# Optimization experiments

Hardware: AMD Instinct MI355X
Metric: run time of the kernel (lower is better)

## Reference

```python
import jax, jax.numpy as jnp
import numpy as np

NEG = -9.0e15
D = 768


def _init_params(key, d):
    ks = jax.random.split(key, 12)
    s = 0.02
    p = {}
    p['Wa'] = jax.random.normal(ks[0], (d, 1), jnp.float32) * s
    p['ba'] = jnp.zeros((1,), jnp.float32)
    for i, name in enumerate(['qs', 'ks', 'qc', 'kc', 'qr', 'kr']):
        p['W' + name] = jax.random.normal(ks[1 + i], (d, d), jnp.float32) * s
        p['b' + name] = jnp.zeros((d,), jnp.float32)
    p['Wf1'] = jax.random.normal(ks[8], (3 * d, d), jnp.float32) * s
    p['bf1'] = jnp.zeros((d,), jnp.float32)
    p['Wf2'] = jax.random.normal(ks[9], (d, d), jnp.float32) * s
    p['bf2'] = jnp.zeros((d,), jnp.float32)
    p['gamma'] = jnp.ones((d,), jnp.float32)
    p['beta'] = jnp.zeros((d,), jnp.float32)
    return p


def setup_inputs() -> dict:
    key = jax.random.key(0)
    k1, k2, k3 = jax.random.split(key, 3)
    B, L = 8, 1024
    inp = {
        'x': jax.random.normal(k1, (B, L, D), jnp.float32),
        'x_ids': jax.random.randint(k2, (B, L), 0, 1000, jnp.int64 if jax.config.read('jax_enable_x64') else jnp.int32).astype(jnp.int32),
        'pad_idx': 0,
    }
    inp.update(_init_params(k3, D))
    return inp


def _forward(x, x_ids, pad_idx, Wa, ba, Wqs, bqs, Wks, bks, Wqc, bqc, Wkc, bkc,
             Wqr, bqr, Wkr, bkr, Wf1, bf1, Wf2, bf2, gamma, beta):
    B, L, d = x.shape
    valid = x_ids != pad_idx                             # [B,L]
    valid_len = valid.sum(axis=1)
    sep_pos = jnp.clip(valid_len // 2, 1, max(1, L - 2))  # [B]
    pos = jnp.arange(L)[None, :]                          # [1,L]
    false_mask = (pos < sep_pos[:, None]) & valid         # [B,L]
    option_mask = (pos > sep_pos[:, None]) & valid        # [B,L]

    # anomaly gate over false segment
    a_logits = (x @ Wa + ba)[..., 0]                      # [B,L]
    a_logits = jnp.where(false_mask, a_logits, NEG)
    gate = jax.nn.softmax(a_logits, axis=1) * false_mask.astype(x.dtype)
    gate = gate / jnp.clip(gate.sum(axis=1, keepdims=True), 1e-8)

    scale = 1.0 / jnp.sqrt(jnp.asarray(d, x.dtype))
    q_sup, k_sup = x @ Wqs + bqs, x @ Wks + bks
    q_con, k_con = x @ Wqc + bqc, x @ Wkc + bkc
    q_rep, k_rep = x @ Wqr + bqr, x @ Wkr + bkr

    sup_s = jnp.einsum('bld,bmd->blm', q_sup, k_sup) * scale
    con_s = jnp.einsum('bld,bmd->blm', q_con, k_con) * scale
    rep_s = jnp.einsum('bld,bmd->blm', q_rep, k_rep) * scale

    pair_mask = false_mask[:, :, None] & option_mask[:, None, :]  # [B,L,L]
    sup_attn = jax.nn.softmax(jnp.where(pair_mask, sup_s, NEG), axis=-1)
    rep_attn = jax.nn.softmax(jnp.where(pair_mask, rep_s + jnp.tanh(con_s), NEG), axis=-1)

    rep_vec = jnp.einsum('blm,bmd->bld', rep_attn, x)
    sup_vec = jnp.einsum('blm,bmd->bld', sup_attn, x)

    anomaly_false = jnp.einsum('bl,bld->bd', gate, x)
    w_rep = jnp.einsum('bl,bld->bd', gate, rep_vec)
    w_sup = jnp.einsum('bl,bld->bd', gate, sup_vec)

    fused = jnp.concatenate([anomaly_false, w_rep, w_sup], axis=-1)
    fused = jnp.maximum(fused @ Wf1 + bf1, 0.0) @ Wf2 + bf2  # dropout = eval identity

    mu = fused.mean(axis=-1, keepdims=True)
    var = ((fused - mu) ** 2).mean(axis=-1, keepdims=True)
    fused = (fused - mu) / jnp.sqrt(var + 1e-5) * gamma + beta
    return fused


def reference(x, x_ids, pad_idx, Wa, ba, Wqs, bqs, Wks, bks, Wqc, bqc, Wkc, bkc,
              Wqr, bqr, Wkr, bkr, Wf1, bf1, Wf2, bf2, gamma, beta):
    return _forward(x, x_ids, pad_idx, Wa, ba, Wqs, bqs, Wks, bks, Wqc, bqc,
                    Wkc, bkc, Wqr, bqr, Wkr, bkr, Wf1, bf1, Wf2, bf2, gamma, beta)
```

## Files before the change

### kernel.cpp

```cpp
#include <hip/hip_runtime.h>
#include <math.h>

#define L 1024
#define NB 8
#define D 768
#define NEGV (-9.0e15f)
#define SCALE 0.036084391824351615f

typedef unsigned short u16;
typedef __attribute__((ext_vector_type(8))) short short8;
typedef __attribute__((ext_vector_type(4))) float float4v;
#define MFMA_BF16 __builtin_amdgcn_mfma_f32_16x16x32_bf16

__device__ __forceinline__ float b2f(u16 u) {
    union { unsigned int i; float f; } v; v.i = ((unsigned int)u) << 16; return v.f;
}
__device__ __forceinline__ u16 f2b(float f) {
    union { float fv; unsigned int i; } v; v.fv = f;
    unsigned int x = v.i;
    x += 0x7fffu + ((x >> 16) & 1u);
    return (u16)(x >> 16);
}
__device__ __forceinline__ float unpk(unsigned int w, int h) {
    return b2f((u16)(h ? (w >> 16) : (w & 0xffffu)));
}

template<int F32>
__device__ __forceinline__ float4 ld4(const void* p, size_t idx) {
    if (F32) return *(const float4*)((const float*)p + idx);
    ushort4 v = *(const ushort4*)((const u16*)p + idx);
    return make_float4(b2f(v.x), b2f(v.y), b2f(v.z), b2f(v.w));
}
template<int F32>
__device__ __forceinline__ float ld1(const void* p, size_t idx) {
    if (F32) return ((const float*)p)[idx];
    return b2f(((const u16*)p)[idx]);
}
__device__ __forceinline__ int ldid(const int* p, size_t idx, int is64) {
    return is64 ? p[idx * 2] : p[idx];
}

__device__ __forceinline__ void detect2(const void* x, const void* ids, int* sh) {
    int tid = threadIdx.x;
    if (tid < 64) {
        u16 u = ((const u16*)x)[tid * 2];
        int e = (u >> 7) & 0xFF;
        unsigned long long balf = __ballot(e >= 100 && e <= 140);
        int v = ((const int*)ids)[tid * 2 + 1];
        unsigned long long bali = __ballot(v != 0);
        if (tid == 0) {
            sh[0] = (__popcll(balf) < 32) ? 1 : 0;
            sh[1] = (bali == 0ULL) ? 1 : 0;
        }
    }
    __syncthreads();
}

#define WS_FLAG  ((size_t)0)
#define WS_SEP   ((size_t)64)
#define WS_C0    ((size_t)128)
#define WS_Z0    ((size_t)192)
#define WS_W1    ((size_t)9472)
#define WS_GATE  ((size_t)18752)
#define WS_CSUP  ((size_t)51520)
#define WS_CREP  ((size_t)84288)
#define WS_AF    ((size_t)117056)
#define WS_WREP  ((size_t)141632)
#define WS_WSUP  ((size_t)166208)
#define WS_HACC  ((size_t)190784)
#define WS_ALOG  ((size_t)215360)
#define WS_T     ((size_t)248128)
#define WS_OACC  ((size_t)303104)
#define WS_XB    ((size_t)524288)
#define WS_Z     ((size_t)13107200)
#define WS_WB    ((size_t)31981568)
#define WS_M     ((size_t)40370176)

struct PP { const void* W[6]; const void* b[6]; };

template<int F32> __device__ void kbias_body(const void* W, const void* vec,
        float* out, float* vs, int xi) {
    int tid = threadIdx.x;
    for (int i = tid; i < D; i += 256) vs[i] = ld1<F32>(vec, i);
    __syncthreads();
    int row = xi * 64 + (tid >> 2);
    int sub = tid & 3;
    float acc = 0.f;
    for (int i = 0; i < 48; ++i) {
        int k = i * 16 + sub * 4;
        float4 wv = ld4<F32>(W, (size_t)row * D + k);
        acc += wv.x * vs[k] + wv.y * vs[k + 1] + wv.z * vs[k + 2] + wv.w * vs[k + 3];
    }
    acc += __shfl_xor(acc, 1);
    acc += __shfl_xor(acc, 2);
    if (sub == 0) out[row] = acc;
}
template<int F32> __device__ void kc0_body(const void* bq, const void* bk,
        float* c0, float* red) {
    int tid = threadIdx.x;
    float s = 0.f;
    for (int i = tid; i < D; i += 256) s += ld1<F32>(bq, i) * ld1<F32>(bk, i);
    red[tid] = s; __syncthreads();
    for (int st = 128; st > 0; st >>= 1) { if (tid < st) red[tid] += red[tid + st]; __syncthreads(); }
    if (tid == 0) c0[0] = red[0];
}

template<int F32> __device__ void kx_body(const void* x, const void* Wa,
        const void* ba, u16* xb, float* alog, float* ws2) {
    int tid = threadIdx.x;
    for (int i = tid; i < D; i += 256) ws2[i] = ld1<F32>(Wa, i);
    __syncthreads();
    int row = blockIdx.x * 32 + (tid >> 3);
    int sub = tid & 7;
    float a0 = 0.f;
    for (int i = 0; i < 24; ++i) {
        int k = i * 32 + sub * 4;
        float4 xv = ld4<F32>(x, (size_t)row * D + k);
        ushort4 o;
        o.x = f2b(xv.x); o.y = f2b(xv.y); o.z = f2b(xv.z); o.w = f2b(xv.w);
        *(ushort4*)(xb + (size_t)row * D + k) = o;
        a0 += xv.x * ws2[k] + xv.y * ws2[k + 1] + xv.z * ws2[k + 2] + xv.w * ws2[k + 3];
    }
    #pragma unroll
    for (int d = 1; d < 8; d <<= 1) a0 += __shfl_xor(a0, d);
    if (sub == 0) alog[row] = a0 + ld1<F32>(ba, 0);
}
__global__ __launch_bounds__(256) void kx(const void* x, const int* ids, PP pp,
        const void* Wa, const void* ba, u16* xb, u16* Wb, float* alog,
        float* z0, float* w1, float* c0f) {
    __shared__ float sf[2 * D];
    __shared__ int fsh[2];
    detect2(x, ids, fsh);
    int F32 = fsh[0];
    int bid = blockIdx.x;
    if (bid < 256) {
        if (F32) kx_body<1>(x, Wa, ba, xb, alog, sf);
        else     kx_body<0>(x, Wa, ba, xb, alog, sf);
        return;
    }
    if (bid < 1984) {
        int t = (bid - 256) / 288, inner = (bid - 256) % 288;
        const void* src = pp.W[t];
        u16* dst = Wb + (size_t)t * D * D;
        size_t base = ((size_t)inner * 256 + threadIdx.x) * 8;
        if (F32) {
            float4 a = *(const float4*)((const float*)src + base);
            float4 b = *(const float4*)((const float*)src + base + 4);
            uint4 o; u16* po = (u16*)&o;
            po[0] = f2b(a.x); po[1] = f2b(a.y); po[2] = f2b(a.z); po[3] = f2b(a.w);
            po[4] = f2b(b.x); po[5] = f2b(b.y); po[6] = f2b(b.z); po[7] = f2b(b.w);
            *(uint4*)(dst + base) = o;
        } else {
            *(uint4*)(dst + base) = *(const uint4*)((const u16*)src + base);
        }
        return;
    }
    int i = bid - 1984;
    int y = i / 12, xi = i % 12;
    float* vs = sf;
    float* red = sf + D;
    if (y == 4) {
        if (xi != 0) return;
        if (F32) kc0_body<1>(pp.b[2], pp.b[3], c0f, red);
        else     kc0_body<0>(pp.b[2], pp.b[3], c0f, red);
        return;
    }
    const void* W; const void* vec; float* out;
    if (y < 3) { W = pp.W[2 * y + 1]; vec = pp.b[2 * y]; out = z0 + y * D; }
    else       { W = pp.W[2];         vec = pp.b[3];     out = w1; }
    if (F32) kbias_body<1>(W, vec, out, vs, xi);
    else     kbias_body<0>(W, vec, out, vs, xi);
}

__device__ __forceinline__ void stage128_async(const u16* __restrict__ G, size_t ld,
        int r0, int k0, u16* S, int tid) {
    int rowa = tid >> 2;
    int koa = ((tid & 3) ^ (rowa & 3)) << 3;
    int wave = tid >> 6;
    const u16* g1 = &G[(size_t)(r0 + rowa) * ld + k0 + koa];
    const u16* g2 = &G[(size_t)(r0 + rowa + 64) * ld + k0 + koa];
    __builtin_amdgcn_global_load_lds((__attribute__((address_space(1))) void*)(u16*)g1,
        (__attribute__((address_space(3))) void*)(S + wave * 512), 16, 0, 0);
    __builtin_amdgcn_global_load_lds((__attribute__((address_space(1))) void*)(u16*)g2,
        (__attribute__((address_space(3))) void*)(S + 2048 + wave * 512), 16, 0, 0);
}
__device__ __forceinline__ void stage64_async(const u16* __restrict__ G, size_t ld,
        int r0, int k0, u16* S, int tid) {
    int rowa = tid >> 2;
    int koa = ((tid & 3) ^ (rowa & 3)) << 3;
    int wave = tid >> 6;
    const u16* g = &G[(size_t)(r0 + rowa) * ld + k0 + koa];
    __builtin_amdgcn_global_load_lds((__attribute__((address_space(1))) void*)(u16*)g,
        (__attribute__((address_space(3))) void*)(S + wave * 512), 16, 0, 0);
}

__device__ __forceinline__ void gemm64_cnt(const u16* __restrict__ A, size_t lda, int r0,
        const u16* __restrict__ B, size_t ldb, int c0,
        u16* As, u16* Bs, float4v acc[2][4]) {
    int tid = threadIdx.x;
    int lane = tid & 63, wave = tid >> 6;
    int wm = (wave >> 1) << 5, wn = (wave & 1) << 6;
    int quad = lane >> 4, lrow = lane & 15;
    int sq = ((quad ^ (lrow & 3)) << 3);
    #pragma unroll
    for (int i = 0; i < 2; ++i)
        #pragma unroll
        for (int j = 0; j < 4; ++j) acc[i][j] = (float4v){0.f, 0.f, 0.f, 0.f};
    stage64_async(A, lda, r0, 0, As, tid);
    stage64_async(A, lda, r0, 32, As + 2048, tid);
    stage128_async(B, ldb, c0, 0, Bs, tid);
    stage128_async(B, ldb, c0, 32, Bs + 4096, tid);
    stage64_async(A, lda, r0, 64, As + 4096, tid);
    stage64_async(A, lda, r0, 96, As + 6144, tid);
    stage128_async(B, ldb, c0, 64, Bs + 8192, tid);
    stage128_async(B, ldb, c0, 96, Bs + 12288, tid);
    #pragma unroll 1
    for (int t = 0; t < 12; ++t) {
        int cur = t & 1;
        if (t != 11) asm volatile("s_waitcnt vmcnt(6)" ::: "memory");
        else         asm volatile("s_waitcnt vmcnt(0)" ::: "memory");
        __builtin_amdgcn_s_barrier();
        const u16* Ab = As + cur * 4096;
        const u16* Bb = Bs + cur * 8192;
        short8 fa[2][2], fb[2][4];
        #pragma unroll
        for (int p = 0; p < 2; ++p) {
            #pragma unroll
            for (int i = 0; i < 2; ++i)
                fa[p][i] = *(const short8*)&Ab[p * 2048 + (wm + i * 16 + lrow) * 32 + sq];
            #pragma unroll
            for (int j = 0; j < 4; ++j)
                fb[p][j] = *(const short8*)&Bb[p * 4096 + (wn + j * 16 + lrow) * 32 + sq];
        }
        asm volatile("s_waitcnt lgkmcnt(0)" ::: "memory");
        __builtin_amdgcn_sched_barrier(0);
        __builtin_amdgcn_s_barrier();
        if (t < 10) {
            int k0 = (t + 2) << 6;
            u16* Ad = As + cur * 4096;
            u16* Bd = Bs + cur * 8192;
            stage64_async(A, lda, r0, k0, Ad, tid);
            stage64_async(A, lda, r0, k0 + 32, Ad + 2048, tid);
            stage128_async(B, ldb, c0, k0, Bd, tid);
            stage128_async(B, ldb, c0, k0 + 32, Bd + 4096, tid);
        }
        #pragma unroll
        for (int p = 0; p < 2; ++p)
            #pragma unroll
            for (int i = 0; i < 2; ++i)
                #pragma unroll
                for (int j = 0; j < 4; ++j)
                    acc[i][j] = MFMA_BF16(fa[p][i], fb[p][j], acc[i][j], 0, 0, 0);
    }
}

__device__ __forceinline__ void gemm128_cnt(const u16* __restrict__ A, size_t lda, int r0,
        const u16* __restrict__ B, size_t ldb, int c0,
        u16* As, u16* Bs, float4v acc[4][4]) {
    int tid = threadIdx.x;
    int lane = tid & 63, wave = tid >> 6;
    int wm = (wave >> 1) << 6, wn = (wave & 1) << 6;
    int quad = lane >> 4, lrow = lane & 15;
    int sq = ((quad ^ (lrow & 3)) << 3);
    #pragma unroll
    for (int i = 0; i < 4; ++i)
        #pragma unroll
        for (int j = 0; j < 4; ++j) acc[i][j] = (float4v){0.f, 0.f, 0.f, 0.f};
    stage128_async(A, lda, r0, 0, As, tid);
    stage128_async(A, lda, r0, 32, As + 4096, tid);
    stage128_async(B, ldb, c0, 0, Bs, tid);
    stage128_async(B, ldb, c0, 32, Bs + 4096, tid);
    stage128_async(A, lda, r0, 64, As + 8192, tid);
    stage128_async(A, lda, r0, 96, As + 12288, tid);
    stage128_async(B, ldb, c0, 64, Bs + 8192, tid);
    stage128_async(B, ldb, c0, 96, Bs + 12288, tid);
    #pragma unroll 1
    for (int t = 0; t < 12; ++t) {
        int cur = t & 1;
        if (t != 11) asm volatile("s_waitcnt vmcnt(8)" ::: "memory");
        else         asm volatile("s_waitcnt vmcnt(0)" ::: "memory");
        __builtin_amdgcn_s_barrier();
        const u16* Ab = As + cur * 8192;
        const u16* Bb = Bs + cur * 8192;
        short8 fa[2][4], fb[2][4];
        #pragma unroll
        for (int p = 0; p < 2; ++p) {
            #pragma unroll
            for (int i = 0; i < 4; ++i)
                fa[p][i] = *(const short8*)&Ab[p * 4096 + (wm + i * 16 + lrow) * 32 + sq];
            #pragma unroll
            for (int j = 0; j < 4; ++j)
                fb[p][j] = *(const short8*)&Bb[p * 4096 + (wn + j * 16 + lrow) * 32 + sq];
        }
        asm volatile("s_waitcnt lgkmcnt(0)" ::: "memory");
        __builtin_amdgcn_sched_barrier(0);
        __builtin_amdgcn_s_barrier();
        if (t < 10) {
            int k0 = (t + 2) << 6;
            u16* Ad = As + cur * 8192;
            u16* Bd = Bs + cur * 8192;
            stage128_async(A, lda, r0, k0, Ad, tid);
            stage128_async(A, lda, r0, k0 + 32, Ad + 4096, tid);
            stage128_async(B, ldb, c0, k0, Bd, tid);
            stage128_async(B, ldb, c0, k0 + 32, Bd + 4096, tid);
        }
        #pragma unroll
        for (int p = 0; p < 2; ++p)
            #pragma unroll
            for (int i = 0; i < 4; ++i)
                #pragma unroll
                for (int j = 0; j < 4; ++j)
                    acc[i][j] = MFMA_BF16(fa[p][i], fb[p][j], acc[i][j], 0, 0, 0);
    }
}

__global__ __launch_bounds__(256) void kB(const void* x, const int* __restrict__ ids,
        const int* __restrict__ padp, const float* __restrict__ alog,
        float* __restrict__ gate, int* __restrict__ sepArr,
        float* __restrict__ af, float* __restrict__ wrep, float* __restrict__ wsup,
        float* __restrict__ hacc, float* __restrict__ oacc,
        float* __restrict__ csup, float* __restrict__ crep,
        const u16* __restrict__ xb, const float* __restrict__ w1,
        const float* __restrict__ c0f, float* __restrict__ tbuf,
        const u16* __restrict__ Wb, u16* __restrict__ Mt) {
    __shared__ __align__(16) u16 SMEM[24576];
    int bid = blockIdx.x;
    int tid = threadIdx.x;
    if (bid >= 8 && bid < 224) {
        int i = bid - 8;
        int p = i / 72, j = i % 72;
        int r0 = (j / 6) * 64, c0m = (j % 6) * 128;
        u16* As = SMEM;
        u16* Bs = SMEM + 8192;
        float4v acc[2][4];
        gemm64_cnt(Wb + (size_t)(2 * p + 1) * D * D, D, r0,
                   Wb + (size_t)(2 * p) * D * D, D, c0m, As, Bs, acc);
        int lane = tid & 63, wave = tid >> 6;
        int wm = (wave >> 1) << 5, wn = (wave & 1) << 6;
        int quad = lane >> 4, lrow = lane & 15;
        u16* out = Mt + (size_t)p * D * D;
        #pragma unroll
        for (int ii = 0; ii < 2; ++ii)
            #pragma unroll
            for (int jj = 0; jj < 4; ++jj) {
                int brow = r0 + wm + ii * 16 + quad * 4;
                int col = c0m + wn + jj * 16 + lrow;
                #pragma unroll
                for (int r = 0; r < 4; ++r)
                    out[(size_t)(brow + r) * D + col] = f2b(acc[ii][jj][r]);
            }
        return;
    }
    if (bid >= 224) {
        int i = bid - 224;
        int b = i >> 2, q = i & 3;
        float* w1s = (float*)SMEM;
        for (int j = tid; j < D; j += 256) w1s[j] = w1[j];
        __syncthreads();
        float c0v = c0f[0];
        int sub = tid & 15;
        int rowi = tid >> 4;
        for (int pass = 0; pass < 8; ++pass) {
            int l = q * 128 + pass * 16 + rowi;
            const u16* xr = xb + ((size_t)b * L + l) * D;
            float a = 0.f;
            #pragma unroll
            for (int i2 = 0; i2 < 6; ++i2) {
                int k = i2 * 128 + sub * 8;
                short8 v = *(const short8*)&xr[k];
                #pragma unroll
                for (int e = 0; e < 8; ++e) a += b2f((u16)v[e]) * w1s[k + e];
            }
            #pragma unroll
            for (int d2 = 1; d2 < 16; d2 <<= 1) a += __shfl_xor(a, d2);
            if (sub == 0) tbuf[b * 512 + l] = a + c0v;
        }
        return;
    }
    float* red = (float*)SMEM;
    int*   ish = (int*)(red + 256);
    detect2(x, ids, ish);
    int is64 = ish[1];
    int b = bid;
    int pad = padp[0];
    int cnt = 0;
    for (int l = tid; l < L; l += 256) cnt += (ldid(ids, (size_t)b * L + l, is64) != pad) ? 1 : 0;
    red[tid] = (float)cnt; __syncthreads();
    for (int s = 128; s > 0; s >>= 1) { if (tid < s) red[tid] += red[tid + s]; __syncthreads(); }
    if (tid == 0) {
        int vl = (int)red[0];
        int sep = vl / 2; if (sep < 1) sep = 1; if (sep > L - 2) sep = L - 2;
        ish[2] = sep; sepArr[b] = sep;
    }
    __syncthreads();
    int sep = ish[2];
    float lv[4]; int lidx[4];
    float mx = -3.4e38f;
    for (int u = 0; u < 4; ++u) {
        int l = tid + u * 256; lidx[u] = l;
        bool fm = (l < sep) && (ldid(ids, (size_t)b * L + l, is64) != pad);
        float v = fm ? alog[b * L + l] : NEGV;
        lv[u] = v; mx = fmaxf(mx, v);
    }
    red[tid] = mx; __syncthreads();
    for (int s = 128; s > 0; s >>= 1) { if (tid < s) red[tid] = fmaxf(red[tid], red[tid + s]); __syncthreads(); }
    mx = red[0]; __syncthreads();
    float se = 0.f;
    for (int u = 0; u < 4; ++u) { lv[u] = expf(lv[u] - mx); se += lv[u]; }
    red[tid] = se; __syncthreads();
    for (int s = 128; s > 0; s >>= 1) { if (tid < s) red[tid] += red[tid + s]; __syncthreads(); }
    float den = fmaxf(red[0], 1e-30f); __syncthreads();
    float gs = 0.f; float gv[4];
    for (int u = 0; u < 4; ++u) {
        int l = lidx[u];
        bool fm = (l < sep) && (ldid(ids, (size_t)b * L + l, is64) != pad);
        float p = lv[u] / den;
        gv[u] = fm ? p : 0.f;
        gs += gv[u];
    }
    red[tid] = gs; __syncthreads();
    for (int s = 128; s > 0; s >>= 1) { if (tid < s) red[tid] += red[tid + s]; __syncthreads(); }
    gs = red[0];
    float inv = 1.f / fmaxf(gs, 1e-8f);
    for (int u = 0; u < 4; ++u) gate[b * L + lidx[u]] = gv[u] * inv;
    for (int l = tid; l < L; l += 256) { csup[b * L + l] = 0.f; crep[b * L + l] = 0.f; }
    for (int i = tid; i < D; i += 256) {
        af[b * D + i] = 0.f; wrep[b * D + i] = 0.f; wsup[b * D + i] = 0.f;
        hacc[b * D + i] = 0.f; oacc[b * D + i] = 0.f;
    }
}

__global__ __launch_bounds__(256) void kZ_mfma(const u16* __restrict__ xb,
        const u16* __restrict__ Mt, const float* __restrict__ z0,
        u16* __restrict__ Zbuf, const int* __restrict__ sepArr) {
    __shared__ __align__(16) u16 As[16384];
    __shared__ __align__(16) u16 Bs[16384];
    int z = blockIdx.z;
    int p = z >> 3, b = z & 7;
    int sep = sepArr[b];
    int r0 = blockIdx.y * 128;
    if (r0 >= sep) return;
    int c0 = blockIdx.x * 128;
    float4v acc[4][4];
    gemm128_cnt(xb + (size_t)b * L * D, D, r0,
                Mt + (size_t)p * D * D, D, c0, As, Bs, acc);
    int lane = threadIdx.x & 63, wave = threadIdx.x >> 6;
    int wm = (wave >> 1) << 6, wn = (wave & 1) << 6;
    int quad = lane >> 4, lrow = lane & 15;
    const float* z0p = z0 + p * D;
    u16* out = Zbuf + ((size_t)p * NB + b) * 512 * D;
    #pragma unroll
    for (int i = 0; i < 4; ++i)
        #pragma unroll
        for (int j = 0; j < 4; ++j) {
            int brow = r0 + wm + i * 16 + quad * 4;
            int col = c0 + wn + j * 16 + lrow;
            float zb = z0p[col];
            #pragma unroll
            for (int r = 0; r < 4; ++r)
                out[(size_t)(brow + r) * D + col] = f2b(acc[i][j][r] + zb);
        }
}

__global__ __launch_bounds__(512) void kS2(const u16* __restrict__ Zbuf,
        const u16* __restrict__ xb, const float* __restrict__ tcbuf,
        const int* __restrict__ sepArr, const int* __restrict__ ids,
        const int* __restrict__ padp, const float* __restrict__ gate,
        float* __restrict__ csup, float* __restrict__ crep) {
    __shared__ __align__(16) u16 Alds[24576];
    __shared__ float redmx[2][8][16];
    __shared__ float redsm[2][8][16];
    __shared__ int ish[1];
    int bid = blockIdx.x;
    int b = bid & 7;
    int l0 = (bid >> 3) * 16;
    int sep = sepArr[b];
    int tid = threadIdx.x, lane = tid & 63, wave = tid >> 6;
    int lrow = lane & 15, quad = lane >> 4;
    if (tid < 64) {
        int v = ((const int*)ids)[tid * 2 + 1];
        unsigned long long bali = __ballot(v != 0);
        if (tid == 0) ish[0] = (bali == 0ULL) ? 1 : 0;
    }
    __syncthreads();
    if (l0 >= sep) return;
    int is64 = ish[0];
    int pad = padp[0];
    int msta = ((sep + 1) >> 7) << 7;
    int nchunk = (L - msta) >> 7;
    const u16* A0 = Zbuf + (size_t)b * 512 * D;
    const u16* A1 = Zbuf + ((size_t)NB + b) * 512 * D;
    const u16* A2 = Zbuf + ((size_t)2 * NB + b) * 512 * D;
    const u16* X  = xb + (size_t)b * L * D;
    #pragma unroll
    for (int i = 0; i < 6; ++i) {
        int s = tid + i * 512;
        int m = s / 1536, rem = s - m * 1536;
        int r = rem / 96, c = rem - r * 96;
        const u16* src = (m == 0 ? A1 : A2) + (size_t)(l0 + r) * D + c * 8;
        *(short8*)&Alds[(((m * 16 + r) * 96) + (c ^ (r & 7))) * 8] = *(const short8*)src;
    }
    __syncthreads();
    float tcv[4], gr[4];
    #pragma unroll
    for (int r = 0; r < 4; ++r) {
        tcv[r] = tcbuf[b * 512 + l0 + quad * 4 + r];
        gr[r]  = gate[b * L + l0 + quad * 4 + r];
    }
    int xr = lrow & 7;
    int arow0 = lrow * 768;
    const u16* pA0_ = A0 + (size_t)(l0 + lrow) * D + quad * 8;
    unsigned int pS[8][2], pC[8][2];
    #pragma unroll
    for (int g = 0; g < 2; ++g) {
      if (g * 4 < nchunk) {
        const u16 *pB0_, *pB1_, *pB2_, *pB3_;
        {
            int m00 = msta + (g * 4 + 0) * 128; if (m00 > L - 128) m00 = L - 128;
            int m01 = msta + (g * 4 + 1) * 128; if (m01 > L - 128) m01 = L - 128;
            int m02 = msta + (g * 4 + 2) * 128; if (m02 > L - 128) m02 = L - 128;
            int m03 = msta + (g * 4 + 3) * 128; if (m03 > L - 128) m03 = L - 128;
            pB0_ = X + (size_t)(m00 + wave * 16 + lrow) * D + quad * 8;
            pB1_ = X + (size_t)(m01 + wave * 16 + lrow) * D + quad * 8;
            pB2_ = X + (size_t)(m02 + wave * 16 + lrow) * D + quad * 8;
            pB3_ = X + (size_t)(m03 + wave * 16 + lrow) * D + quad * 8;
        }
        float4v acc[3][4];
        #pragma unroll
        for (int m = 0; m < 3; ++m)
            #pragma unroll
            for (int cc = 0; cc < 4; ++cc) acc[m][cc] = (float4v){0.f, 0.f, 0.f, 0.f};
        short8 fA1, fA2;
        short8 A0a, B0a, B1a, B2a, B3a;
        short8 A0b, B0b, B1b, B2b, B3b;
        short8 A0c, B0c, B1c, B2c, B3c;
#define GL_(dst, base, imm) asm volatile("global_load_dwordx4 %0, %1, off offset:" #imm : "=v"(dst) : "v"(base))
#define GL(dst, base, imm) GL_(dst, base, imm)
#define LDG5(SUF, IMM) do { \
        GL(A0##SUF, pA0_, IMM); \
        GL(B0##SUF, pB0_, IMM); GL(B1##SUF, pB1_, IMM); \
        GL(B2##SUF, pB2_, IMM); GL(B3##SUF, pB3_, IMM); } while (0)
#define LDA(S) do { int sw = (((4 * (S) + quad) ^ xr) << 3); \
        fA1 = *(const short8*)&Alds[arow0 + sw]; \
        fA2 = *(const short8*)&Alds[12288 + arow0 + sw]; } while (0)
#define WAITN_(N) do { asm volatile("s_waitcnt vmcnt(" #N ")"); \
        __builtin_amdgcn_sched_barrier(0); } while (0)
#define WAITN(N) WAITN_(N)
#define CPSTEP(SUF) do { \
        acc[0][0] = MFMA_BF16(A0##SUF, B0##SUF, acc[0][0], 0, 0, 0); \
        acc[1][0] = MFMA_BF16(fA1, B0##SUF, acc[1][0], 0, 0, 0); \
        acc[2][0] = MFMA_BF16(fA2, B0##SUF, acc[2][0], 0, 0, 0); \
        acc[0][1] = MFMA_BF16(A0##SUF, B1##SUF, acc[0][1], 0, 0, 0); \
        acc[1][1] = MFMA_BF16(fA1, B1##SUF, acc[1][1], 0, 0, 0); \
        acc[2][1] = MFMA_BF16(fA2, B1##SUF, acc[2][1], 0, 0, 0); \
        acc[0][2] = MFMA_BF16(A0##SUF, B2##SUF, acc[0][2], 0, 0, 0); \
        acc[1][2] = MFMA_BF16(fA1, B2##SUF, acc[1][2], 0, 0, 0); \
        acc[2][2] = MFMA_BF16(fA2, B2##SUF, acc[2][2], 0, 0, 0); \
        acc[0][3] = MFMA_BF16(A0##SUF, B3##SUF, acc[0][3], 0, 0, 0); \
        acc[1][3] = MFMA_BF16(fA1, B3##SUF, acc[1][3], 0, 0, 0); \
        acc[2][3] = MFMA_BF16(fA2, B3##SUF, acc[2][3], 0, 0, 0); } while (0)
        WAITN(0);
        LDG5(a, 0); LDG5(b, 64); LDG5(c, 128);
        LDA(0);  WAITN(10); CPSTEP(a); LDG5(a, 192);
        LDA(1);  WAITN(10); CPSTEP(b); LDG5(b, 256);
        LDA(2);  WAITN(10); CPSTEP(c); LDG5(c, 320);
        LDA(3);  WAITN(10); CPSTEP(a); LDG5(a, 384);
        LDA(4);  WAITN(10); CPSTEP(b); LDG5(b, 448);
        LDA(5);  WAITN(10); CPSTEP(c); LDG5(c, 512);
        LDA(6);  WAITN(10); CPSTEP(a); LDG5(a, 576);
        LDA(7);  WAITN(10); CPSTEP(b); LDG5(b, 640);
        LDA(8);  WAITN(10); CPSTEP(c); LDG5(c, 704);
        LDA(9);  WAITN(10); CPSTEP(a); LDG5(a, 768);
        LDA(10); WAITN(10); CPSTEP(b); LDG5(b, 832);
        LDA(11); WAITN(10); CPSTEP(c); LDG5(c, 896);
        LDA(12); WAITN(10); CPSTEP(a); LDG5(a, 960);
        LDA(13); WAITN(10); CPSTEP(b); LDG5(b, 1024);
        LDA(14); WAITN(10); CPSTEP(c); LDG5(c, 1088);
        LDA(15); WAITN(10); CPSTEP(a); LDG5(a, 1152);
        LDA(16); WAITN(10); CPSTEP(b); LDG5(b, 1216);
        LDA(17); WAITN(10); CPSTEP(c); LDG5(c, 1280);
        LDA(18); WAITN(10); CPSTEP(a); LDG5(a, 1344);
        LDA(19); WAITN(10); CPSTEP(b); LDG5(b, 1408);
        LDA(20); WAITN(10); CPSTEP(c); LDG5(c, 1472);
        LDA(21); WAITN(10); CPSTEP(a);
        LDA(22); WAITN(5);  CPSTEP(b);
        LDA(23); WAITN(0);  CPSTEP(c);
#undef GL_
#undef GL
#undef LDG5
#undef LDA
#undef WAITN_
#undef WAITN
#undef CPSTEP
        #pragma unroll
        for (int cc = 0; cc < 4; ++cc) {
            int c = g * 4 + cc;
            if (c < nchunk) {
                int m = msta + c * 128 + wave * 16 + lrow;
                bool ok = (m > sep) && (ldid(ids, (size_t)b * L + m, is64) != pad);
                float vs[4], vc[4];
                #pragma unroll
                for (int r = 0; r < 4; ++r) {
                    vs[r] = ok ? acc[0][cc][r] * SCALE : NEGV;
                    vc[r] = ok ? (acc[2][cc][r] * SCALE
                                  + tanhf((acc[1][cc][r] + tcv[r]) * SCALE)) : NEGV;
                }
                pS[c][0] = (unsigned)f2b(vs[0]) | ((unsigned)f2b(vs[1]) << 16);
                pS[c][1] = (unsigned)f2b(vs[2]) | ((unsigned)f2b(vs[3]) << 16);
                pC[c][0] = (unsigned)f2b(vc[0]) | ((unsigned)f2b(vc[1]) << 16);
                pC[c][1] = (unsigned)f2b(vc[2]) | ((unsigned)f2b(vc[3]) << 16);
            }
        }
      }
    }
    float mxs[4], mxc[4];
    #pragma unroll
    for (int r = 0; r < 4; ++r) { mxs[r] = -3.4e38f; mxc[r] = -3.4e38f; }
    #pragma unroll
    for (int c = 0; c < 8; ++c) if (c < nchunk)
        #pragma unroll
        for (int r = 0; r < 4; ++r) {
            mxs[r] = fmaxf(mxs[r], unpk(pS[c][r >> 1], r & 1));
            mxc[r] = fmaxf(mxc[r], unpk(pC[c][r >> 1], r & 1));
        }
    #pragma unroll
    for (int d = 1; d < 16; d <<= 1)
        #pragma unroll
        for (int r = 0; r < 4; ++r) {
            mxs[r] = fmaxf(mxs[r], __shfl_xor(mxs[r], d));
            mxc[r] = fmaxf(mxc[r], __shfl_xor(mxc[r], d));
        }
    if (lrow == 0)
        #pragma unroll
        for (int r = 0; r < 4; ++r) {
            redmx[0][wave][quad * 4 + r] = mxs[r];
            redmx[1][wave][quad * 4 + r] = mxc[r];
        }
    __syncthreads();
    #pragma unroll
    for (int r = 0; r < 4; ++r) {
        int rr = quad * 4 + r;
        float m0 = redmx[0][0][rr], m1 = redmx[1][0][rr];
        #pragma unroll
        for (int w = 1; w < 8; ++w) {
            m0 = fmaxf(m0, redmx[0][w][rr]);
            m1 = fmaxf(m1, redmx[1][w][rr]);
        }
        mxs[r] = m0; mxc[r] = m1;
    }
    float sms[4], smc[4];
    #pragma unroll
    for (int r = 0; r < 4; ++r) { sms[r] = 0.f; smc[r] = 0.f; }
    #pragma unroll
    for (int c = 0; c < 8; ++c) if (c < nchunk)
        #pragma unroll
        for (int r = 0; r < 4; ++r) {
            sms[r] += expf(unpk(pS[c][r >> 1], r & 1) - mxs[r]);
            smc[r] += expf(unpk(pC[c][r >> 1], r & 1) - mxc[r]);
        }
    #pragma unroll
    for (int d = 1; d < 16; d <<= 1)
        #pragma unroll
        for (int r = 0; r < 4; ++r) {
            sms[r] += __shfl_xor(sms[r], d);
            smc[r] += __shfl_xor(smc[r], d);
        }
    if (lrow == 0)
        #pragma unroll
        for (int r = 0; r < 4; ++r) {
            redsm[0][wave][quad * 4 + r] = sms[r];
            redsm[1][wave][quad * 4 + r] = smc[r];
        }
    __syncthreads();
    float wgs[4], wgc[4];
    #pragma unroll
    for (int r = 0; r < 4; ++r) {
        int rr = quad * 4 + r;
        float d0 = redsm[0][0][rr], d1 = redsm[1][0][rr];
        #pragma unroll
        for (int w = 1; w < 8; ++w) {
            d0 += redsm[0][w][rr];
            d1 += redsm[1][w][rr];
        }
        wgs[r] = gr[r] / fmaxf(d0, 1e-30f);
        wgc[r] = gr[r] / fmaxf(d1, 1e-30f);
    }
    #pragma unroll
    for (int c = 0; c < 8; ++c) if (c < nchunk) {
        float as = 0.f, ar = 0.f;
        #pragma unroll
        for (int r = 0; r < 4; ++r) {
            as += wgs[r] * expf(unpk(pS[c][r >> 1], r & 1) - mxs[r]);
            ar += wgc[r] * expf(unpk(pC[c][r >> 1], r & 1) - mxc[r]);
        }
        as += __shfl_xor(as, 16); as += __shfl_xor(as, 32);
        ar += __shfl_xor(ar, 16); ar += __shfl_xor(ar, 32);
        if (quad == 0) {
            int m = msta + c * 128 + wave * 16 + lrow;
            atomicAdd(&csup[b * L + m], as);
            atomicAdd(&crep[b * L + m], ar);
        }
    }
}

__global__ __launch_bounds__(256) void k3(const u16* __restrict__ xb,
        const float* __restrict__ gate, const float* __restrict__ csup,
        const float* __restrict__ crep, float* __restrict__ af,
        float* __restrict__ wrep, float* __restrict__ wsup) {
    int b = blockIdx.y, c = blockIdx.x;
    int tid = threadIdx.x;
    float a0 = 0.f, a1 = 0.f, a2 = 0.f;
    float r0 = 0.f, r1 = 0.f, r2 = 0.f;
    float q0 = 0.f, q1 = 0.f, q2 = 0.f;
    for (int mm = 0; mm < 16; ++mm) {
        int m = c * 16 + mm;
        float wg = gate[b * L + m], wr = crep[b * L + m], wq = csup[b * L + m];
        if (wg == 0.f && wr == 0.f && wq == 0.f) continue;
        size_t base = ((size_t)b * L + m) * D;
        float x0 = b2f(xb[base + tid]);
        float x1 = b2f(xb[base + tid + 256]);
        float x2 = b2f(xb[base + tid + 512]);
        a0 += wg * x0; a1 += wg * x1; a2 += wg * x2;
        r0 += wr * x0; r1 += wr * x1; r2 += wr * x2;
        q0 += wq * x0; q1 += wq * x1; q2 += wq * x2;
    }
    atomicAdd(&af[b * D + tid], a0); atomicAdd(&af[b * D + tid + 256], a1); atomicAdd(&af[b * D + tid + 512], a2);
    atomicAdd(&wrep[b * D + tid], r0); atomicAdd(&wrep[b * D + tid + 256], r1); atomicAdd(&wrep[b * D + tid + 512], r2);
    atomicAdd(&wsup[b * D + tid], q0); atomicAdd(&wsup[b * D + tid + 256], q1); atomicAdd(&wsup[b * D + tid + 512], q2);
}

template<int F32> __device__ void kh1_body(const float* af, const float* wrep,
        const float* wsup, const void* Wf1, float* hacc, float* fs) {
    int tid = threadIdx.x;
    int c0 = blockIdx.x * 128, k0 = blockIdx.y * 144;
    for (int e = tid; e < 8 * 144; e += 256) {
        int b = e / 144, kk = e - b * 144;
        int k = k0 + kk;
        float v = (k < D) ? af[b * D + k] : (k < 2 * D) ? wrep[b * D + k - D]
                                                        : wsup[b * D + k - 2 * D];
        fs[b * 144 + kk] = v;
    }
    __syncthreads();
    int col = c0 + (tid & 127);
    int kg = tid >> 7;
    float acc[NB];
    #pragma unroll
    for (int b = 0; b < NB; ++b) acc[b] = 0.f;
    #pragma unroll 4
    for (int r = 0; r < 72; ++r) {
        int kk = kg * 72 + r;
        float w = ld1<F32>(Wf1, (size_t)(k0 + kk) * D + col);
        #pragma unroll
        for (int b = 0; b < NB; ++b) acc[b] += fs[b * 144 + kk] * w;
    }
    #pragma unroll
    for (int b = 0; b < NB; ++b) atomicAdd(&hacc[b * D + col], acc[b]);
}
__global__ __launch_bounds__(256) void kh1(const void* x, const int* ids,
        const float* af, const float* wrep,
        const float* wsup, const void* Wf1, float* hacc) {
    __shared__ float fs[8 * 144];
    __shared__ int fsh[2];
    detect2(x, ids, fsh);
    if (fsh[0]) kh1_body<1>(af, wrep, wsup, Wf1, hacc, fs);
    else        kh1_body<0>(af, wrep, wsup, Wf1, hacc, fs);
}

template<int F32> __device__ void kh2_body(const float* hacc, const void* bf1,
        const void* Wf2, float* oacc, float* hsl) {
    int tid = threadIdx.x;
    int c0 = blockIdx.x * 128, k0 = blockIdx.y * 96;
    for (int e = tid; e < 8 * 96; e += 256) {
        int b = e / 96, kk = e - b * 96;
        int k = k0 + kk;
        hsl[b * 96 + kk] = fmaxf(hacc[b * D + k] + ld1<F32>(bf1, k), 0.f);
    }
    __syncthreads();
    int col = c0 + (tid & 127);
    int kg = tid >> 7;
    float acc[NB];
    #pragma unroll
    for (int b = 0; b < NB; ++b) acc[b] = 0.f;
    #pragma unroll 4
    for (int r = 0; r < 48; ++r) {
        int kk = kg * 48 + r;
        float w = ld1<F32>(Wf2, (size_t)(k0 + kk) * D + col);
        #pragma unroll
        for (int b = 0; b < NB; ++b) acc[b] += hsl[b * 96 + kk] * w;
    }
    #pragma unroll
    for (int b = 0; b < NB; ++b) atomicAdd(&oacc[b * D + col], acc[b]);
}
__global__ __launch_bounds__(256) void kh2(const void* x, const int* ids,
        const float* hacc, const void* bf1,
        const void* Wf2, float* oacc) {
    __shared__ float hsl[8 * 96];
    __shared__ int fsh[2];
    detect2(x, ids, fsh);
    if (fsh[0]) kh2_body<1>(hacc, bf1, Wf2, oacc, hsl);
    else        kh2_body<0>(hacc, bf1, Wf2, oacc, hsl);
}

template<int F32> __device__ void kln_body(const float* oacc, const void* bf2,
        const void* gamma, const void* beta, void* out, float* red) {
    int b = blockIdx.x, tid = threadIdx.x;
    float o[3];
    #pragma unroll
    for (int u = 0; u < 3; ++u) {
        int i = tid + u * 256;
        o[u] = oacc[b * D + i] + ld1<F32>(bf2, i);
    }
    red[tid] = o[0] + o[1] + o[2]; __syncthreads();
    for (int s = 128; s > 0; s >>= 1) { if (tid < s) red[tid] += red[tid + s]; __syncthreads(); }
    float mu = red[0] / (float)D; __syncthreads();
    float vs = 0.f;
    #pragma unroll
    for (int u = 0; u < 3; ++u) vs += (o[u] - mu) * (o[u] - mu);
    red[tid] = vs; __syncthreads();
    for (int s = 128; s > 0; s >>= 1) { if (tid < s) red[tid] += red[tid + s]; __syncthreads(); }
    float var = red[0] / (float)D;
    float rstd = 1.0f / sqrtf(var + 1e-5f);
    #pragma unroll
    for (int u = 0; u < 3; ++u) {
        int i = tid + u * 256;
        float v = (o[u] - mu) * rstd * ld1<F32>(gamma, i) + ld1<F32>(beta, i);
        if (F32) ((float*)out)[b * D + i] = v;
        else     ((u16*)out)[b * D + i] = f2b(v);
    }
}
__global__ __launch_bounds__(256) void kln(const void* x, const int* ids,
        const float* oacc, const void* bf2,
        const void* gamma, const void* beta, void* out) {
    __shared__ float red[256];
    __shared__ int fsh[2];
    detect2(x, ids, fsh);
    if (fsh[0]) kln_body<1>(oacc, bf2, gamma, beta, out, red);
    else        kln_body<0>(oacc, bf2, gamma, beta, out, red);
}

extern "C" void kernel_launch(void* const* d_in, const int* in_sizes, int n_in,
                              void* d_out, int out_size, void* d_ws, size_t ws_size,
                              hipStream_t stream) {
    const void* x    = d_in[0];
    const int* ids   = (const int*)d_in[1];
    const int* padp  = (const int*)d_in[2];
    const void* Wa   = d_in[3];
    const void* ba   = d_in[4];
    PP pp;
    pp.W[0] = d_in[5];  pp.b[0] = d_in[6];
    pp.W[1] = d_in[7];  pp.b[1] = d_in[8];
    pp.W[2] = d_in[9];  pp.b[2] = d_in[10];
    pp.W[3] = d_in[11]; pp.b[3] = d_in[12];
    pp.W[4] = d_in[13]; pp.b[4] = d_in[14];
    pp.W[5] = d_in[15]; pp.b[5] = d_in[16];
    const void* Wf1 = d_in[17]; const void* bf1 = d_in[18];
    const void* Wf2 = d_in[19]; const void* bf2 = d_in[20];
    const void* gamma = d_in[21]; const void* beta = d_in[22];

    char* ws = (char*)d_ws;
    int*   sepArr = (int*)(ws + WS_SEP);
    float* c0   = (float*)(ws + WS_C0);
    float* z0   = (float*)(ws + WS_Z0);
    float* w1   = (float*)(ws + WS_W1);
    float* gate = (float*)(ws + WS_GATE);
    float* csup = (float*)(ws + WS_CSUP);
    float* crep = (float*)(ws + WS_CREP);
    float* af   = (float*)(ws + WS_AF);
    float* wrep = (float*)(ws + WS_WREP);
    float* wsup = (float*)(ws + WS_WSUP);
    float* hacc = (float*)(ws + WS_HACC);
    float* oacc = (float*)(ws + WS_OACC);
    float* alog = (float*)(ws + WS_ALOG);
    float* tbuf = (float*)(ws + WS_T);
    u16* xb   = (u16*)(ws + WS_XB);
    u16* Zbuf = (u16*)(ws + WS_Z);
    u16* Wb   = (u16*)(ws + WS_WB);
    u16* Mt   = (u16*)(ws + WS_M);

    kx<<<dim3(2044), dim3(256), 0, stream>>>(x, ids, pp, Wa, ba, xb, Wb, alog, z0, w1, c0);
    kB<<<dim3(256), dim3(256), 0, stream>>>(x, ids, padp, alog, gate, sepArr,
                                            af, wrep, wsup, hacc, oacc, csup, crep,
                                            xb, w1, c0, tbuf, Wb, Mt);
    kZ_mfma<<<dim3(6, 4, 24), dim3(256), 0, stream>>>(xb, Mt, z0, Zbuf, sepArr);
    kS2<<<dim3(256), dim3(512), 0, stream>>>(Zbuf, xb, tbuf, sepArr, ids, padp,
                                             gate, csup, crep);
    k3<<<dim3(64, NB), dim3(256), 0, stream>>>(xb, gate, csup, crep, af, wrep, wsup);
    kh1<<<dim3(6, 16), dim3(256), 0, stream>>>(x, ids, af, wrep, wsup, Wf1, hacc);
    kh2<<<dim3(6, 8), dim3(256), 0, stream>>>(x, ids, hacc, bf1, Wf2, oacc);
    kln<<<dim3(NB), dim3(256), 0, stream>>>(x, ids, oacc, bf2, gamma, beta, d_out);
}
```

Baseline: 252.4 us.

## Split kS2 key columns across 16 waves with 1024-thread blocks

The score kernel kS2 goes from 8 waves each handling four 16-key column tiles per pass to 16 waves each handling two 16-key tiles per pass. The flat pair index maps each wave to its tiles, empty slots are filled with a masked negative constant, and the cross-wave max and sum reductions are widened to 16 entries. The aim is more waves in flight per block and fewer registers per wave, to hide the latency of global B-loads. In exchange, the A0 fragments are loaded from global by twice as many waves, and the larger block may limit how many blocks fit on a compute unit.

```diff
diff --git a/kernel.cpp b/kernel.cpp
--- a/kernel.cpp
+++ b/kernel.cpp
@@ -462,14 +462,14 @@
         }
 }
 
-__global__ __launch_bounds__(512) void kS2(const u16* __restrict__ Zbuf,
+__global__ __launch_bounds__(1024) void kS2(const u16* __restrict__ Zbuf,
         const u16* __restrict__ xb, const float* __restrict__ tcbuf,
         const int* __restrict__ sepArr, const int* __restrict__ ids,
         const int* __restrict__ padp, const float* __restrict__ gate,
         float* __restrict__ csup, float* __restrict__ crep) {
     __shared__ __align__(16) u16 Alds[24576];
-    __shared__ float redmx[2][8][16];
-    __shared__ float redsm[2][8][16];
+    __shared__ float redmx[2][16][16];
+    __shared__ float redsm[2][16][16];
     __shared__ int ish[1];
     int bid = blockIdx.x;
     int b = bid & 7;
@@ -488,13 +488,14 @@
     int pad = padp[0];
     int msta = ((sep + 1) >> 7) << 7;
     int nchunk = (L - msta) >> 7;
+    int npairs = nchunk * 8;
     const u16* A0 = Zbuf + (size_t)b * 512 * D;
     const u16* A1 = Zbuf + ((size_t)NB + b) * 512 * D;
     const u16* A2 = Zbuf + ((size_t)2 * NB + b) * 512 * D;
     const u16* X  = xb + (size_t)b * L * D;
     #pragma unroll
-    for (int i = 0; i < 6; ++i) {
-        int s = tid + i * 512;
+    for (int i = 0; i < 3; ++i) {
+        int s = tid + i * 1024;
         int m = s / 1536, rem = s - m * 1536;
         int r = rem / 96, c = rem - r * 96;
         const u16* src = (m == 0 ? A1 : A2) + (size_t)(l0 + r) * D + c * 8;
@@ -510,36 +511,31 @@
     int xr = lrow & 7;
     int arow0 = lrow * 768;
     const u16* pA0_ = A0 + (size_t)(l0 + lrow) * D + quad * 8;
-    unsigned int pS[8][2], pC[8][2];
-    #pragma unroll
-    for (int g = 0; g < 2; ++g) {
-      if (g * 4 < nchunk) {
-        const u16 *pB0_, *pB1_, *pB2_, *pB3_;
-        {
-            int m00 = msta + (g * 4 + 0) * 128; if (m00 > L - 128) m00 = L - 128;
-            int m01 = msta + (g * 4 + 1) * 128; if (m01 > L - 128) m01 = L - 128;
-            int m02 = msta + (g * 4 + 2) * 128; if (m02 > L - 128) m02 = L - 128;
-            int m03 = msta + (g * 4 + 3) * 128; if (m03 > L - 128) m03 = L - 128;
-            pB0_ = X + (size_t)(m00 + wave * 16 + lrow) * D + quad * 8;
-            pB1_ = X + (size_t)(m01 + wave * 16 + lrow) * D + quad * 8;
-            pB2_ = X + (size_t)(m02 + wave * 16 + lrow) * D + quad * 8;
-            pB3_ = X + (size_t)(m03 + wave * 16 + lrow) * D + quad * 8;
-        }
-        float4v acc[3][4];
+    const unsigned NEGP = (unsigned)f2b(NEGV) | ((unsigned)f2b(NEGV) << 16);
+    unsigned int pS[4][2], pC[4][2];
+    #pragma unroll
+    for (int pass = 0; pass < 2; ++pass) {
+      if (pass * 32 < npairs) {
+        int p0 = pass * 32 + wave * 2;
+        int p1 = p0 + 1;
+        int r0a = msta + (p0 >> 3) * 128 + (p0 & 7) * 16; if (r0a > L - 16) r0a = L - 16;
+        int r1a = msta + (p1 >> 3) * 128 + (p1 & 7) * 16; if (r1a > L - 16) r1a = L - 16;
+        const u16* pB0_ = X + (size_t)(r0a + lrow) * D + quad * 8;
+        const u16* pB1_ = X + (size_t)(r1a + lrow) * D + quad * 8;
+        float4v acc[3][2];
         #pragma unroll
         for (int m = 0; m < 3; ++m)
             #pragma unroll
-            for (int cc = 0; cc < 4; ++cc) acc[m][cc] = (float4v){0.f, 0.f, 0.f, 0.f};
+            for (int s2 = 0; s2 < 2; ++s2) acc[m][s2] = (float4v){0.f, 0.f, 0.f, 0.f};
         short8 fA1, fA2;
-        short8 A0a, B0a, B1a, B2a, B3a;
-        short8 A0b, B0b, B1b, B2b, B3b;
-        short8 A0c, B0c, B1c, B2c, B3c;
+        short8 A0a, B0a, B1a;
+        short8 A0b, B0b, B1b;
+        short8 A0c, B0c, B1c;
 #define GL_(dst, base, imm) asm volatile("global_load_dwordx4 %0, %1, off offset:" #imm : "=v"(dst) : "v"(base))
 #define GL(dst, base, imm) GL_(dst, base, imm)
-#define LDG5(SUF, IMM) do { \
+#define LDG3(SUF, IMM) do { \
         GL(A0##SUF, pA0_, IMM); \
-        GL(B0##SUF, pB0_, IMM); GL(B1##SUF, pB1_, IMM); \
-        GL(B2##SUF, pB2_, IMM); GL(B3##SUF, pB3_, IMM); } while (0)
+        GL(B0##SUF, pB0_, IMM); GL(B1##SUF, pB1_, IMM); } while (0)
 #define LDA(S) do { int sw = (((4 * (S) + quad) ^ xr) << 3); \
         fA1 = *(const short8*)&Alds[arow0 + sw]; \
         fA2 = *(const short8*)&Alds[12288 + arow0 + sw]; } while (0)
@@ -552,64 +548,63 @@
         acc[2][0] = MFMA_BF16(fA2, B0##SUF, acc[2][0], 0, 0, 0); \
         acc[0][1] = MFMA_BF16(A0##SUF, B1##SUF, acc[0][1], 0, 0, 0); \
         acc[1][1] = MFMA_BF16(fA1, B1##SUF, acc[1][1], 0, 0, 0); \
-        acc[2][1] = MFMA_BF16(fA2, B1##SUF, acc[2][1], 0, 0, 0); \
-        acc[0][2] = MFMA_BF16(A0##SUF, B2##SUF, acc[0][2], 0, 0, 0); \
-        acc[1][2] = MFMA_BF16(fA1, B2##SUF, acc[1][2], 0, 0, 0); \
-        acc[2][2] = MFMA_BF16(fA2, B2##SUF, acc[2][2], 0, 0, 0); \
-        acc[0][3] = MFMA_BF16(A0##SUF, B3##SUF, acc[0][3], 0, 0, 0); \
-        acc[1][3] = MFMA_BF16(fA1, B3##SUF, acc[1][3], 0, 0, 0); \
-        acc[2][3] = MFMA_BF16(fA2, B3##SUF, acc[2][3], 0, 0, 0); } while (0)
+        acc[2][1] = MFMA_BF16(fA2, B1##SUF, acc[2][1], 0, 0, 0); } while (0)
         WAITN(0);
-        LDG5(a, 0); LDG5(b, 64); LDG5(c, 128);
-        LDA(0);  WAITN(10); CPSTEP(a); LDG5(a, 192);
-        LDA(1);  WAITN(10); CPSTEP(b); LDG5(b, 256);
-        LDA(2);  WAITN(10); CPSTEP(c); LDG5(c, 320);
-        LDA(3);  WAITN(10); CPSTEP(a); LDG5(a, 384);
-        LDA(4);  WAITN(10); CPSTEP(b); LDG5(b, 448);
-        LDA(5);  WAITN(10); CPSTEP(c); LDG5(c, 512);
-        LDA(6);  WAITN(10); CPSTEP(a); LDG5(a, 576);
-        LDA(7);  WAITN(10); CPSTEP(b); LDG5(b, 640);
-        LDA(8);  WAITN(10); CPSTEP(c); LDG5(c, 704);
-        LDA(9);  WAITN(10); CPSTEP(a); LDG5(a, 768);
-        LDA(10); WAITN(10); CPSTEP(b); LDG5(b, 832);
-        LDA(11); WAITN(10); CPSTEP(c); LDG5(c, 896);
-        LDA(12); WAITN(10); CPSTEP(a); LDG5(a, 960);
-        LDA(13); WAITN(10); CPSTEP(b); LDG5(b, 1024);
-        LDA(14); WAITN(10); CPSTEP(c); LDG5(c, 1088);
-        LDA(15); WAITN(10); CPSTEP(a); LDG5(a, 1152);
-        LDA(16); WAITN(10); CPSTEP(b); LDG5(b, 1216);
-        LDA(17); WAITN(10); CPSTEP(c); LDG5(c, 1280);
-        LDA(18); WAITN(10); CPSTEP(a); LDG5(a, 1344);
-        LDA(19); WAITN(10); CPSTEP(b); LDG5(b, 1408);
-        LDA(20); WAITN(10); CPSTEP(c); LDG5(c, 1472);
-        LDA(21); WAITN(10); CPSTEP(a);
-        LDA(22); WAITN(5);  CPSTEP(b);
-        LDA(23); WAITN(0);  CPSTEP(c);
+        LDG3(a, 0); LDG3(b, 64); LDG3(c, 128);
+        LDA(0);  WAITN(6); CPSTEP(a); LDG3(a, 192);
+        LDA(1);  WAITN(6); CPSTEP(b); LDG3(b, 256);
+        LDA(2);  WAITN(6); CPSTEP(c); LDG3(c, 320);
+        LDA(3);  WAITN(6); CPSTEP(a); LDG3(a, 384);
+        LDA(4);  WAITN(6); CPSTEP(b); LDG3(b, 448);
+        LDA(5);  WAITN(6); CPSTEP(c); LDG3(c, 512);
+        LDA(6);  WAITN(6); CPSTEP(a); LDG3(a, 576);
+        LDA(7);  WAITN(6); CPSTEP(b); LDG3(b, 640);
+        LDA(8);  WAITN(6); CPSTEP(c); LDG3(c, 704);
+        LDA(9);  WAITN(6); CPSTEP(a); LDG3(a, 768);
+        LDA(10); WAITN(6); CPSTEP(b); LDG3(b, 832);
+        LDA(11); WAITN(6); CPSTEP(c); LDG3(c, 896);
+        LDA(12); WAITN(6); CPSTEP(a); LDG3(a, 960);
+        LDA(13); WAITN(6); CPSTEP(b); LDG3(b, 1024);
+        LDA(14); WAITN(6); CPSTEP(c); LDG3(c, 1088);
+        LDA(15); WAITN(6); CPSTEP(a); LDG3(a, 1152);
+        LDA(16); WAITN(6); CPSTEP(b); LDG3(b, 1216);
+        LDA(17); WAITN(6); CPSTEP(c); LDG3(c, 1280);
+        LDA(18); WAITN(6); CPSTEP(a); LDG3(a, 1344);
+        LDA(19); WAITN(6); CPSTEP(b); LDG3(b, 1408);
+        LDA(20); WAITN(6); CPSTEP(c); LDG3(c, 1472);
+        LDA(21); WAITN(6); CPSTEP(a);
+        LDA(22); WAITN(3); CPSTEP(b);
+        LDA(23); WAITN(0); CPSTEP(c);
 #undef GL_
 #undef GL
-#undef LDG5
+#undef LDG3
 #undef LDA
 #undef WAITN_
 #undef WAITN
 #undef CPSTEP
         #pragma unroll
-        for (int cc = 0; cc < 4; ++cc) {
-            int c = g * 4 + cc;
-            if (c < nchunk) {
-                int m = msta + c * 128 + wave * 16 + lrow;
-                bool ok = (m > sep) && (ldid(ids, (size_t)b * L + m, is64) != pad);
-                float vs[4], vc[4];
-                #pragma unroll
-                for (int r = 0; r < 4; ++r) {
-                    vs[r] = ok ? acc[0][cc][r] * SCALE : NEGV;
-                    vc[r] = ok ? (acc[2][cc][r] * SCALE
-                                  + tanhf((acc[1][cc][r] + tcv[r]) * SCALE)) : NEGV;
-                }
-                pS[c][0] = (unsigned)f2b(vs[0]) | ((unsigned)f2b(vs[1]) << 16);
-                pS[c][1] = (unsigned)f2b(vs[2]) | ((unsigned)f2b(vs[3]) << 16);
-                pC[c][0] = (unsigned)f2b(vc[0]) | ((unsigned)f2b(vc[1]) << 16);
-                pC[c][1] = (unsigned)f2b(vc[2]) | ((unsigned)f2b(vc[3]) << 16);
+        for (int s2 = 0; s2 < 2; ++s2) {
+            int pr = p0 + s2;
+            int m = msta + (pr >> 3) * 128 + (pr & 7) * 16 + lrow;
+            bool ok = (pr < npairs) && (m > sep) && (m < L)
+                      && (ldid(ids, (size_t)b * L + m, is64) != pad);
+            float vs[4], vc[4];
+            #pragma unroll
+            for (int r = 0; r < 4; ++r) {
+                vs[r] = ok ? acc[0][s2][r] * SCALE : NEGV;
+                vc[r] = ok ? (acc[2][s2][r] * SCALE
+                              + tanhf((acc[1][s2][r] + tcv[r]) * SCALE)) : NEGV;
             }
+            pS[pass * 2 + s2][0] = (unsigned)f2b(vs[0]) | ((unsigned)f2b(vs[1]) << 16);
+            pS[pass * 2 + s2][1] = (unsigned)f2b(vs[2]) | ((unsigned)f2b(vs[3]) << 16);
+            pC[pass * 2 + s2][0] = (unsigned)f2b(vc[0]) | ((unsigned)f2b(vc[1]) << 16);
+            pC[pass * 2 + s2][1] = (unsigned)f2b(vc[2]) | ((unsigned)f2b(vc[3]) << 16);
+        }
+      } else {
+        #pragma unroll
+        for (int s2 = 0; s2 < 2; ++s2) {
+            pS[pass * 2 + s2][0] = NEGP; pS[pass * 2 + s2][1] = NEGP;
+            pC[pass * 2 + s2][0] = NEGP; pC[pass * 2 + s2][1] = NEGP;
         }
       }
     }
@@ -617,11 +612,11 @@
     #pragma unroll
     for (int r = 0; r < 4; ++r) { mxs[r] = -3.4e38f; mxc[r] = -3.4e38f; }
     #pragma unroll
-    for (int c = 0; c < 8; ++c) if (c < nchunk)
+    for (int ps = 0; ps < 4; ++ps)
         #pragma unroll
         for (int r = 0; r < 4; ++r) {
-            mxs[r] = fmaxf(mxs[r], unpk(pS[c][r >> 1], r & 1));
-            mxc[r] = fmaxf(mxc[r], unpk(pC[c][r >> 1], r & 1));
+            mxs[r] = fmaxf(mxs[r], unpk(pS[ps][r >> 1], r & 1));
+            mxc[r] = fmaxf(mxc[r], unpk(pC[ps][r >> 1], r & 1));
         }
     #pragma unroll
     for (int d = 1; d < 16; d <<= 1)
@@ -642,7 +637,7 @@
         int rr = quad * 4 + r;
         float m0 = redmx[0][0][rr], m1 = redmx[1][0][rr];
         #pragma unroll
-        for (int w = 1; w < 8; ++w) {
+        for (int w = 1; w < 16; ++w) {
             m0 = fmaxf(m0, redmx[0][w][rr]);
             m1 = fmaxf(m1, redmx[1][w][rr]);
         }
@@ -652,11 +647,11 @@
     #pragma unroll
     for (int r = 0; r < 4; ++r) { sms[r] = 0.f; smc[r] = 0.f; }
     #pragma unroll
-    for (int c = 0; c < 8; ++c) if (c < nchunk)
+    for (int ps = 0; ps < 4; ++ps)
         #pragma unroll
         for (int r = 0; r < 4; ++r) {
-            sms[r] += expf(unpk(pS[c][r >> 1], r & 1) - mxs[r]);
-            smc[r] += expf(unpk(pC[c][r >> 1], r & 1) - mxc[r]);
+            sms[r] += expf(unpk(pS[ps][r >> 1], r & 1) - mxs[r]);
+            smc[r] += expf(unpk(pC[ps][r >> 1], r & 1) - mxc[r]);
         }
     #pragma unroll
     for (int d = 1; d < 16; d <<= 1)
@@ -678,7 +673,7 @@
         int rr = quad * 4 + r;
         float d0 = redsm[0][0][rr], d1 = redsm[1][0][rr];
         #pragma unroll
-        for (int w = 1; w < 8; ++w) {
+        for (int w = 1; w < 16; ++w) {
             d0 += redsm[0][w][rr];
             d1 += redsm[1][w][rr];
         }
@@ -686,19 +681,22 @@
         wgc[r] = gr[r] / fmaxf(d1, 1e-30f);
     }
     #pragma unroll
-    for (int c = 0; c < 8; ++c) if (c < nchunk) {
-        float as = 0.f, ar = 0.f;
-        #pragma unroll
-        for (int r = 0; r < 4; ++r) {
-            as += wgs[r] * expf(unpk(pS[c][r >> 1], r & 1) - mxs[r]);
-            ar += wgc[r] * expf(unpk(pC[c][r >> 1], r & 1) - mxc[r]);
-        }
-        as += __shfl_xor(as, 16); as += __shfl_xor(as, 32);
-        ar += __shfl_xor(ar, 16); ar += __shfl_xor(ar, 32);
-        if (quad == 0) {
-            int m = msta + c * 128 + wave * 16 + lrow;
-            atomicAdd(&csup[b * L + m], as);
-            atomicAdd(&crep[b * L + m], ar);
+    for (int ps = 0; ps < 4; ++ps) {
+        int pr = (ps >> 1) * 32 + wave * 2 + (ps & 1);
+        if (pr < npairs) {
+            float as = 0.f, ar = 0.f;
+            #pragma unroll
+            for (int r = 0; r < 4; ++r) {
+                as += wgs[r] * expf(unpk(pS[ps][r >> 1], r & 1) - mxs[r]);
+                ar += wgc[r] * expf(unpk(pC[ps][r >> 1], r & 1) - mxc[r]);
+            }
+            as += __shfl_xor(as, 16); as += __shfl_xor(as, 32);
+            ar += __shfl_xor(ar, 16); ar += __shfl_xor(ar, 32);
+            if (quad == 0) {
+                int m = msta + (pr >> 3) * 128 + (pr & 7) * 16 + lrow;
+                atomicAdd(&csup[b * L + m], as);
+                atomicAdd(&crep[b * L + m], ar);
+            }
         }
     }
 }
@@ -882,8 +880,8 @@
                                             af, wrep, wsup, hacc, oacc, csup, crep,
                                             xb, w1, c0, tbuf, Wb, Mt);
     kZ_mfma<<<dim3(6, 4, 24), dim3(256), 0, stream>>>(xb, Mt, z0, Zbuf, sepArr);
-    kS2<<<dim3(256), dim3(512), 0, stream>>>(Zbuf, xb, tbuf, sepArr, ids, padp,
-                                             gate, csup, crep);
+    kS2<<<dim3(256), dim3(1024), 0, stream>>>(Zbuf, xb, tbuf, sepArr, ids, padp,
+                                              gate, csup, crep);
     k3<<<dim3(64, NB), dim3(256), 0, stream>>>(xb, gate, csup, crep, af, wrep, wsup);
     kh1<<<dim3(6, 16), dim3(256), 0, stream>>>(x, ids, af, wrep, wsup, Wf1, hacc);
     kh2<<<dim3(6, 8), dim3(256), 0, stream>>>(x, ids, hacc, bf1, Wf2, oacc);
```

New measurement: 270.5 us. 1.07x slower.
